# Kernel optimization log

Measured on AMD Instinct MI355X. Metric: run time of the kernel, lower is better.

## Reference

```python
import jax, jax.numpy as jnp
import numpy as np

DELTA = 0.2  # margin from __init__
EPS = 1e-8   # torch cosine_similarity eps


def setup_inputs() -> dict:
    key = jax.random.key(0)
    k1, k2, k3 = jax.random.split(key, 3)
    B, D, N = 4096, 1024, 8192
    return {
        "q": jax.random.normal(k1, (B, D), dtype=jnp.float32),
        "k": jax.random.normal(k2, (B, D), dtype=jnp.float32),
        "queue": jax.random.normal(k3, (N, D), dtype=jnp.float32),
    }


def _l2_normalize(x):
    # matches torch cosine_similarity clamping: norm clamped to eps
    n = jnp.maximum(jnp.linalg.norm(x, axis=-1, keepdims=True), EPS)
    return x / n


def reference(q, k, queue):
    qn = _l2_normalize(q)          # [B, D]
    kn = _l2_normalize(k)          # [B, D]
    queuen = _l2_normalize(queue)  # [N, D]
    pos = jnp.sum(qn * kn, axis=-1)                 # [B] cos(q_i, k_i)
    neg = jnp.einsum("bd,nd->bn", qn, queuen)       # [B, N] cos(q_i, queue_j)
    hinge = jax.nn.relu(DELTA - pos[:, None] + neg)  # [B, N]
    return jnp.sum(hinge)
```

## Files before the change

kernel.cpp:

```cpp
#include <hip/hip_runtime.h>

#define B_ROWS 4096
#define N_ROWS 8192
#define DDIM   1024
#define DELTA_M 0.2f
#define EPSF    1e-8f

#define BM 128
#define BN 128
#define BK 32

typedef short bf16x8 __attribute__((ext_vector_type(8)));
typedef float f32x4 __attribute__((ext_vector_type(4)));

__device__ inline unsigned short f32_to_bf16(float f) {
    unsigned int u = __float_as_uint(f);
    u += 0x7FFFu + ((u >> 16) & 1u);
    return (unsigned short)(u >> 16);
}

__device__ inline void load_lds16(const void* g, void* l) {
    __builtin_amdgcn_global_load_lds(
        (const __attribute__((address_space(1))) void*)g,
        (__attribute__((address_space(3))) void*)l,
        16, 0, 0);
}

__global__ __launch_bounds__(256)
void norm_kernel(const float* __restrict__ q, const float* __restrict__ k,
                 const float* __restrict__ queue,
                 unsigned short* __restrict__ qn,
                 unsigned short* __restrict__ qun,
                 float* __restrict__ pos) {
    const int tid  = threadIdx.x;
    const int lane = tid & 63;
    const int wave = tid >> 6;
    const int row  = blockIdx.x * 4 + wave;

    if (row < B_ROWS) {
        const float4* qr = reinterpret_cast<const float4*>(q + (size_t)row * DDIM);
        const float4* kr = reinterpret_cast<const float4*>(k + (size_t)row * DDIM);
        float4 a[4], b[4];
        #pragma unroll
        for (int j = 0; j < 4; ++j) a[j] = qr[lane + j * 64];
        #pragma unroll
        for (int j = 0; j < 4; ++j) b[j] = kr[lane + j * 64];
        float s11 = 0.f, s22 = 0.f, s12 = 0.f;
        #pragma unroll
        for (int j = 0; j < 4; ++j) {
            s11 += a[j].x * a[j].x + a[j].y * a[j].y + a[j].z * a[j].z + a[j].w * a[j].w;
            s22 += b[j].x * b[j].x + b[j].y * b[j].y + b[j].z * b[j].z + b[j].w * b[j].w;
            s12 += a[j].x * b[j].x + a[j].y * b[j].y + a[j].z * b[j].z + a[j].w * b[j].w;
        }
        #pragma unroll
        for (int off = 1; off < 64; off <<= 1) {
            s11 += __shfl_xor(s11, off);
            s22 += __shfl_xor(s22, off);
            s12 += __shfl_xor(s12, off);
        }
        const float inv1 = 1.0f / fmaxf(sqrtf(s11), EPSF);
        const float inv2 = 1.0f / fmaxf(sqrtf(s22), EPSF);
        if (lane == 0) pos[row] = s12 * inv1 * inv2;
        ushort4* orow = reinterpret_cast<ushort4*>(qn + (size_t)row * DDIM);
        #pragma unroll
        for (int j = 0; j < 4; ++j) {
            ushort4 o;
            o.x = f32_to_bf16(a[j].x * inv1);
            o.y = f32_to_bf16(a[j].y * inv1);
            o.z = f32_to_bf16(a[j].z * inv1);
            o.w = f32_to_bf16(a[j].w * inv1);
            orow[lane + j * 64] = o;
        }
    } else {
        const int r2 = row - B_ROWS;
        const float4* qr = reinterpret_cast<const float4*>(queue + (size_t)r2 * DDIM);
        float4 a[4];
        #pragma unroll
        for (int j = 0; j < 4; ++j) a[j] = qr[lane + j * 64];
        float s11 = 0.f;
        #pragma unroll
        for (int j = 0; j < 4; ++j)
            s11 += a[j].x * a[j].x + a[j].y * a[j].y + a[j].z * a[j].z + a[j].w * a[j].w;
        #pragma unroll
        for (int off = 1; off < 64; off <<= 1) s11 += __shfl_xor(s11, off);
        const float inv1 = 1.0f / fmaxf(sqrtf(s11), EPSF);
        ushort4* orow = reinterpret_cast<ushort4*>(qun + (size_t)r2 * DDIM);
        #pragma unroll
        for (int j = 0; j < 4; ++j) {
            ushort4 o;
            o.x = f32_to_bf16(a[j].x * inv1);
            o.y = f32_to_bf16(a[j].y * inv1);
            o.z = f32_to_bf16(a[j].z * inv1);
            o.w = f32_to_bf16(a[j].w * inv1);
            orow[lane + j * 64] = o;
        }
    }
}

__global__ __launch_bounds__(256, 2)
void gemm_hinge(const unsigned short* __restrict__ A,
                const unsigned short* __restrict__ Bq,
                const float* __restrict__ pos,
                float* __restrict__ out) {
    __shared__ unsigned short lA[BM * BK];
    __shared__ unsigned short lB[BN * BK];
    __shared__ float rbuf[4];

    const int tid  = threadIdx.x;
    const int lane = tid & 63;
    const int wave = tid >> 6;

    const int nBM = B_ROWS / BM;
    const int bid = blockIdx.x;
    const int cpx = gridDim.x >> 3;
    const int swz = (bid & 7) * cpx + (bid >> 3);
    const int bm = (swz % nBM) * BM;
    const int bn = (swz / nBM) * BN;

    const int wm = wave >> 1;
    const int wn = wave & 1;

    f32x4 acc[4][4];
    #pragma unroll
    for (int m = 0; m < 4; ++m)
        #pragma unroll
        for (int n = 0; n < 4; ++n)
            acc[m][n] = (f32x4){0.f, 0.f, 0.f, 0.f};

    const int r = tid >> 2;
    const int c = tid & 3;
    const unsigned short* gA0 = A  + (size_t)(bm + r)      * DDIM + c * 8;
    const unsigned short* gA1 = A  + (size_t)(bm + r + 64) * DDIM + c * 8;
    const unsigned short* gB0 = Bq + (size_t)(bn + r)      * DDIM + c * 8;
    const unsigned short* gB1 = Bq + (size_t)(bn + r + 64) * DDIM + c * 8;
    unsigned short* lA0 = lA + tid * 8;
    unsigned short* lA1 = lA + 64 * BK + tid * 8;
    unsigned short* lB0 = lB + tid * 8;
    unsigned short* lB1 = lB + 64 * BK + tid * 8;

    const int arow = wm * 64 + (lane & 15);
    const int brow = wn * 64 + (lane & 15);
    const int kgrp = (lane >> 4) * 8;

    for (int k0 = 0; k0 < DDIM; k0 += BK) {
        load_lds16(gA0 + k0, lA0);
        load_lds16(gA1 + k0, lA1);
        load_lds16(gB0 + k0, lB0);
        load_lds16(gB1 + k0, lB1);
        __syncthreads();
        bf16x8 af[4], bf[4];
        #pragma unroll
        for (int m = 0; m < 4; ++m)
            af[m] = *reinterpret_cast<const bf16x8*>(&lA[(arow + m * 16) * BK + kgrp]);
        #pragma unroll
        for (int n = 0; n < 4; ++n)
            bf[n] = *reinterpret_cast<const bf16x8*>(&lB[(brow + n * 16) * BK + kgrp]);
        #pragma unroll
        for (int m = 0; m < 4; ++m)
            #pragma unroll
            for (int n = 0; n < 4; ++n)
                acc[m][n] = __builtin_amdgcn_mfma_f32_16x16x32_bf16(af[m], bf[n], acc[m][n], 0, 0, 0);
        __syncthreads();
    }

    float lsum = 0.f;
    const int rj = (lane >> 4) << 2;
    #pragma unroll
    for (int m = 0; m < 4; ++m) {
        float p[4];
        #pragma unroll
        for (int j = 0; j < 4; ++j)
            p[j] = pos[bm + wm * 64 + m * 16 + rj + j];
        #pragma unroll
        for (int n = 0; n < 4; ++n)
            #pragma unroll
            for (int j = 0; j < 4; ++j)
                lsum += fmaxf(DELTA_M - p[j] + acc[m][n][j], 0.f);
    }
    #pragma unroll
    for (int off = 32; off; off >>= 1) lsum += __shfl_down(lsum, off);
    if (lane == 0) rbuf[wave] = lsum;
    __syncthreads();
    if (tid == 0) atomicAdd(out, rbuf[0] + rbuf[1] + rbuf[2] + rbuf[3]);
}

extern "C" void kernel_launch(void* const* d_in, const int* in_sizes, int n_in,
                              void* d_out, int out_size, void* d_ws, size_t ws_size,
                              hipStream_t stream) {
    const float* q     = (const float*)d_in[0];
    const float* k     = (const float*)d_in[1];
    const float* queue = (const float*)d_in[2];
    float* out = (float*)d_out;

    unsigned short* qn  = (unsigned short*)d_ws;
    unsigned short* qun = qn + (size_t)B_ROWS * DDIM;
    float* pos = (float*)(qun + (size_t)N_ROWS * DDIM);

    hipMemsetAsync(d_out, 0, sizeof(float), stream);
    norm_kernel<<<(B_ROWS + N_ROWS) / 4, 256, 0, stream>>>(q, k, queue, qn, qun, pos);
    gemm_hinge<<<(B_ROWS / BM) * (N_ROWS / BN), 256, 0, stream>>>(qn, qun, pos, out);
}
```

Before: 183.9 us.

## Double-buffer LDS tiles with global_load_lds prefetch two steps ahead

The GEMM main loop now uses two LDS buffers per operand and issues the global-to-LDS loads for tile t+2 right after the fragments for tile t are read into registers. Explicit vmcnt/lgkmcnt waits and raw s_barrier calls replace the two __syncthreads per iteration, so MFMA work overlaps the next tile's memory traffic. This doubles LDS usage, which could limit occupancy, and the hand-placed waitcnt logic must be exactly right to avoid races.

```diff
diff --git a/kernel.cpp b/kernel.cpp
--- a/kernel.cpp
+++ b/kernel.cpp
@@ -9,6 +9,7 @@
 #define BM 128
 #define BN 128
 #define BK 32
+#define NT (DDIM / BK)
 
 typedef short bf16x8 __attribute__((ext_vector_type(8)));
 typedef float f32x4 __attribute__((ext_vector_type(4)));
@@ -102,8 +103,8 @@
                 const unsigned short* __restrict__ Bq,
                 const float* __restrict__ pos,
                 float* __restrict__ out) {
-    __shared__ unsigned short lA[BM * BK];
-    __shared__ unsigned short lB[BN * BK];
+    __shared__ unsigned short lA[2 * BM * BK];
+    __shared__ unsigned short lB[2 * BN * BK];
     __shared__ float rbuf[4];
 
     const int tid  = threadIdx.x;
@@ -133,34 +134,74 @@
     const unsigned short* gA1 = A  + (size_t)(bm + r + 64) * DDIM + c * 8;
     const unsigned short* gB0 = Bq + (size_t)(bn + r)      * DDIM + c * 8;
     const unsigned short* gB1 = Bq + (size_t)(bn + r + 64) * DDIM + c * 8;
-    unsigned short* lA0 = lA + tid * 8;
-    unsigned short* lA1 = lA + 64 * BK + tid * 8;
-    unsigned short* lB0 = lB + tid * 8;
-    unsigned short* lB1 = lB + 64 * BK + tid * 8;
 
     const int arow = wm * 64 + (lane & 15);
     const int brow = wn * 64 + (lane & 15);
     const int kgrp = (lane >> 4) * 8;
 
-    for (int k0 = 0; k0 < DDIM; k0 += BK) {
-        load_lds16(gA0 + k0, lA0);
-        load_lds16(gA1 + k0, lA1);
-        load_lds16(gB0 + k0, lB0);
-        load_lds16(gB1 + k0, lB1);
-        __syncthreads();
+    {
+        unsigned short* dA = lA;
+        unsigned short* dB = lB;
+        load_lds16(gA0, dA + tid * 8);
+        load_lds16(gA1, dA + 64 * BK + tid * 8);
+        load_lds16(gB0, dB + tid * 8);
+        load_lds16(gB1, dB + 64 * BK + tid * 8);
+        dA = lA + BM * BK;
+        dB = lB + BN * BK;
+        load_lds16(gA0 + BK, dA + tid * 8);
+        load_lds16(gA1 + BK, dA + 64 * BK + tid * 8);
+        load_lds16(gB0 + BK, dB + tid * 8);
+        load_lds16(gB1 + BK, dB + 64 * BK + tid * 8);
+    }
+    asm volatile("s_waitcnt vmcnt(4)" ::: "memory");
+    __builtin_amdgcn_sched_barrier(0);
+    __builtin_amdgcn_s_barrier();
+    __builtin_amdgcn_sched_barrier(0);
+
+    for (int t = 0; t < NT; ++t) {
+        const int cur = t & 1;
+        const unsigned short* lAc = lA + cur * (BM * BK);
+        const unsigned short* lBc = lB + cur * (BN * BK);
+
         bf16x8 af[4], bf[4];
         #pragma unroll
         for (int m = 0; m < 4; ++m)
-            af[m] = *reinterpret_cast<const bf16x8*>(&lA[(arow + m * 16) * BK + kgrp]);
+            af[m] = *reinterpret_cast<const bf16x8*>(&lAc[(arow + m * 16) * BK + kgrp]);
         #pragma unroll
         for (int n = 0; n < 4; ++n)
-            bf[n] = *reinterpret_cast<const bf16x8*>(&lB[(brow + n * 16) * BK + kgrp]);
+            bf[n] = *reinterpret_cast<const bf16x8*>(&lBc[(brow + n * 16) * BK + kgrp]);
+
+        asm volatile("s_waitcnt lgkmcnt(0)" ::: "memory");
+        __builtin_amdgcn_sched_barrier(0);
+        __builtin_amdgcn_s_barrier();
+        __builtin_amdgcn_sched_barrier(0);
+
+        if (t + 2 < NT) {
+            const int k0 = (t + 2) * BK;
+            unsigned short* dA = lA + cur * (BM * BK);
+            unsigned short* dB = lB + cur * (BN * BK);
+            load_lds16(gA0 + k0, dA + tid * 8);
+            load_lds16(gA1 + k0, dA + 64 * BK + tid * 8);
+            load_lds16(gB0 + k0, dB + tid * 8);
+            load_lds16(gB1 + k0, dB + 64 * BK + tid * 8);
+        }
+
         #pragma unroll
         for (int m = 0; m < 4; ++m)
             #pragma unroll
             for (int n = 0; n < 4; ++n)
                 acc[m][n] = __builtin_amdgcn_mfma_f32_16x16x32_bf16(af[m], bf[n], acc[m][n], 0, 0, 0);
-        __syncthreads();
+
+        if (t < NT - 1) {
+            if (t + 2 < NT) {
+                asm volatile("s_waitcnt vmcnt(4)" ::: "memory");
+            } else {
+                asm volatile("s_waitcnt vmcnt(0)" ::: "memory");
+            }
+            __builtin_amdgcn_sched_barrier(0);
+            __builtin_amdgcn_s_barrier();
+            __builtin_amdgcn_sched_barrier(0);
+        }
     }
 
     float lsum = 0.f;
```

After: 179.4 us. 1.02x faster.

## Rewrite GEMM as 256x256 tile, 8-wave, double-buffered pipelined MFMA kernel

Applied to the files above, without the earlier changes.

Replaces the 128x128, single-buffered GEMM with a 256x256 block tile run by 512 threads, each wave computing four sub-quadrants. Global-to-LDS loads are double-buffered over BK=64 and interleaved with MFMA phases, with explicit vmcnt waits, barriers and setprio. LDS addresses get an XOR swizzle to avoid bank conflicts. The aim is more data reuse per load and hiding memory latency behind compute. It needs 128KB of LDS per block, which limits occupancy, and the hand-counted waits are fragile.

```diff
diff --git a/kernel.cpp b/kernel.cpp
--- a/kernel.cpp
+++ b/kernel.cpp
@@ -6,9 +6,8 @@
 #define DELTA_M 0.2f
 #define EPSF    1e-8f
 
-#define BM 128
-#define BN 128
-#define BK 32
+#define BK2 64
+#define NT2 (DDIM / BK2)
 
 typedef short bf16x8 __attribute__((ext_vector_type(8)));
 typedef float f32x4 __attribute__((ext_vector_type(4)));
@@ -24,6 +23,15 @@
         (const __attribute__((address_space(1))) void*)g,
         (__attribute__((address_space(3))) void*)l,
         16, 0, 0);
+}
+
+template<int N> __device__ __forceinline__ void vmwait() {
+    if constexpr (N == 10) asm volatile("s_waitcnt vmcnt(10)" ::: "memory");
+    else if constexpr (N == 8) asm volatile("s_waitcnt vmcnt(8)" ::: "memory");
+    else if constexpr (N == 4) asm volatile("s_waitcnt vmcnt(4)" ::: "memory");
+    else if constexpr (N == 2) asm volatile("s_waitcnt vmcnt(2)" ::: "memory");
+    else asm volatile("s_waitcnt vmcnt(0)" ::: "memory");
+    __builtin_amdgcn_sched_barrier(0);
 }
 
 __global__ __launch_bounds__(256)
@@ -97,91 +105,209 @@
     }
 }
 
-__global__ __launch_bounds__(256, 2)
+__device__ __forceinline__ void stage2(const unsigned short* M, int rowBase, int k0,
+                                       unsigned char* region,
+                                       int sr0, int sc0, int sr1, int sc1, int t16) {
+    load_lds16(M + (size_t)(rowBase + sr0) * DDIM + k0 + sc0, region + t16);
+    load_lds16(M + (size_t)(rowBase + sr1) * DDIM + k0 + sc1, region + 8192 + t16);
+}
+
+template<bool S1, bool S2, int WP0, int WP1, int WNEXT>
+__device__ __forceinline__ void gemm_window(
+    int T, unsigned char* lds,
+    const unsigned short* A, const unsigned short* Bq,
+    int bm, int bn, int wr, int wc, int aLane,
+    int sr0, int sc0, int sr1, int sc1, int t16,
+    f32x4 (&acc)[2][2][4][2]) {
+
+    const int par = T & 1;
+    const int pA0 = par * 32768;
+    const int pA1 = pA0 + 16384;
+    const int pB0 = 65536 + par * 32768;
+    const int pB1 = pB0 + 16384;
+
+    bf16x8 a[4][2], b0[2][2], b1[2][2];
+
+    #pragma unroll
+    for (int fm = 0; fm < 4; ++fm)
+        #pragma unroll
+        for (int ks = 0; ks < 2; ++ks)
+            a[fm][ks] = *reinterpret_cast<const bf16x8*>(
+                &lds[pA0 + wr * 8192 + fm * 2048 + ks * 64 + aLane]);
+    #pragma unroll
+    for (int fn = 0; fn < 2; ++fn)
+        #pragma unroll
+        for (int ks = 0; ks < 2; ++ks)
+            b0[fn][ks] = *reinterpret_cast<const bf16x8*>(
+                &lds[pB0 + wc * 4096 + fn * 2048 + ks * 64 + aLane]);
+    if (S1)
+        stage2(A, bm + 128, (T + 1) * BK2, lds + ((par ^ 1) * 32768 + 16384),
+               sr0, sc0, sr1, sc1, t16);
+    __builtin_amdgcn_s_barrier();
+    asm volatile("s_waitcnt lgkmcnt(0)" ::: "memory");
+    __builtin_amdgcn_sched_barrier(0);
+    __builtin_amdgcn_s_setprio(1);
+    #pragma unroll
+    for (int fm = 0; fm < 4; ++fm)
+        #pragma unroll
+        for (int fn = 0; fn < 2; ++fn)
+            #pragma unroll
+            for (int ks = 0; ks < 2; ++ks)
+                acc[0][0][fm][fn] = __builtin_amdgcn_mfma_f32_16x16x32_bf16(
+                    a[fm][ks], b0[fn][ks], acc[0][0][fm][fn], 0, 0, 0);
+    __builtin_amdgcn_s_setprio(0);
+    vmwait<WP0>();
+    __builtin_amdgcn_s_barrier();
+
+    #pragma unroll
+    for (int fn = 0; fn < 2; ++fn)
+        #pragma unroll
+        for (int ks = 0; ks < 2; ++ks)
+            b1[fn][ks] = *reinterpret_cast<const bf16x8*>(
+                &lds[pB1 + wc * 4096 + fn * 2048 + ks * 64 + aLane]);
+    if (S2)
+        stage2(A, bm, (T + 2) * BK2, lds + pA0, sr0, sc0, sr1, sc1, t16);
+    __builtin_amdgcn_s_barrier();
+    asm volatile("s_waitcnt lgkmcnt(0)" ::: "memory");
+    __builtin_amdgcn_sched_barrier(0);
+    __builtin_amdgcn_s_setprio(1);
+    #pragma unroll
+    for (int fm = 0; fm < 4; ++fm)
+        #pragma unroll
+        for (int fn = 0; fn < 2; ++fn)
+            #pragma unroll
+            for (int ks = 0; ks < 2; ++ks)
+                acc[0][1][fm][fn] = __builtin_amdgcn_mfma_f32_16x16x32_bf16(
+                    a[fm][ks], b1[fn][ks], acc[0][1][fm][fn], 0, 0, 0);
+    __builtin_amdgcn_s_setprio(0);
+    vmwait<WP1>();
+    __builtin_amdgcn_s_barrier();
+
+    #pragma unroll
+    for (int fm = 0; fm < 4; ++fm)
+        #pragma unroll
+        for (int ks = 0; ks < 2; ++ks)
+            a[fm][ks] = *reinterpret_cast<const bf16x8*>(
+                &lds[pA1 + wr * 8192 + fm * 2048 + ks * 64 + aLane]);
+    if (S2)
+        stage2(Bq, bn, (T + 2) * BK2, lds + pB0, sr0, sc0, sr1, sc1, t16);
+    __builtin_amdgcn_s_barrier();
+    asm volatile("s_waitcnt lgkmcnt(0)" ::: "memory");
+    __builtin_amdgcn_sched_barrier(0);
+    __builtin_amdgcn_s_setprio(1);
+    #pragma unroll
+    for (int fm = 0; fm < 4; ++fm)
+        #pragma unroll
+        for (int fn = 0; fn < 2; ++fn)
+            #pragma unroll
+            for (int ks = 0; ks < 2; ++ks)
+                acc[1][1][fm][fn] = __builtin_amdgcn_mfma_f32_16x16x32_bf16(
+                    a[fm][ks], b1[fn][ks], acc[1][1][fm][fn], 0, 0, 0);
+    __builtin_amdgcn_s_setprio(0);
+    __builtin_amdgcn_s_barrier();
+
+    if (S2)
+        stage2(Bq, bn + 128, (T + 2) * BK2, lds + pB1, sr0, sc0, sr1, sc1, t16);
+    __builtin_amdgcn_s_barrier();
+    __builtin_amdgcn_s_setprio(1);
+    #pragma unroll
+    for (int fm = 0; fm < 4; ++fm)
+        #pragma unroll
+        for (int fn = 0; fn < 2; ++fn)
+            #pragma unroll
+            for (int ks = 0; ks < 2; ++ks)
+                acc[1][0][fm][fn] = __builtin_amdgcn_mfma_f32_16x16x32_bf16(
+                    a[fm][ks], b0[fn][ks], acc[1][0][fm][fn], 0, 0, 0);
+    __builtin_amdgcn_s_setprio(0);
+    vmwait<WNEXT>();
+    __builtin_amdgcn_s_barrier();
+}
+
+__global__ __launch_bounds__(512, 2)
 void gemm_hinge(const unsigned short* __restrict__ A,
                 const unsigned short* __restrict__ Bq,
                 const float* __restrict__ pos,
                 float* __restrict__ out) {
-    __shared__ unsigned short lA[BM * BK];
-    __shared__ unsigned short lB[BN * BK];
-    __shared__ float rbuf[4];
+    __shared__ __align__(16) unsigned char lds[131072];
 
     const int tid  = threadIdx.x;
     const int lane = tid & 63;
     const int wave = tid >> 6;
 
-    const int nBM = B_ROWS / BM;
     const int bid = blockIdx.x;
-    const int cpx = gridDim.x >> 3;
-    const int swz = (bid & 7) * cpx + (bid >> 3);
-    const int bm = (swz % nBM) * BM;
-    const int bn = (swz / nBM) * BN;
-
-    const int wm = wave >> 1;
-    const int wn = wave & 1;
-
-    f32x4 acc[4][4];
-    #pragma unroll
-    for (int m = 0; m < 4; ++m)
-        #pragma unroll
-        for (int n = 0; n < 4; ++n)
-            acc[m][n] = (f32x4){0.f, 0.f, 0.f, 0.f};
-
-    const int r = tid >> 2;
-    const int c = tid & 3;
-    const unsigned short* gA0 = A  + (size_t)(bm + r)      * DDIM + c * 8;
-    const unsigned short* gA1 = A  + (size_t)(bm + r + 64) * DDIM + c * 8;
-    const unsigned short* gB0 = Bq + (size_t)(bn + r)      * DDIM + c * 8;
-    const unsigned short* gB1 = Bq + (size_t)(bn + r + 64) * DDIM + c * 8;
-    unsigned short* lA0 = lA + tid * 8;
-    unsigned short* lA1 = lA + 64 * BK + tid * 8;
-    unsigned short* lB0 = lB + tid * 8;
-    unsigned short* lB1 = lB + 64 * BK + tid * 8;
-
-    const int arow = wm * 64 + (lane & 15);
-    const int brow = wn * 64 + (lane & 15);
-    const int kgrp = (lane >> 4) * 8;
-
-    for (int k0 = 0; k0 < DDIM; k0 += BK) {
-        load_lds16(gA0 + k0, lA0);
-        load_lds16(gA1 + k0, lA1);
-        load_lds16(gB0 + k0, lB0);
-        load_lds16(gB1 + k0, lB1);
-        __syncthreads();
-        bf16x8 af[4], bf[4];
-        #pragma unroll
-        for (int m = 0; m < 4; ++m)
-            af[m] = *reinterpret_cast<const bf16x8*>(&lA[(arow + m * 16) * BK + kgrp]);
-        #pragma unroll
-        for (int n = 0; n < 4; ++n)
-            bf[n] = *reinterpret_cast<const bf16x8*>(&lB[(brow + n * 16) * BK + kgrp]);
-        #pragma unroll
-        for (int m = 0; m < 4; ++m)
-            #pragma unroll
-            for (int n = 0; n < 4; ++n)
-                acc[m][n] = __builtin_amdgcn_mfma_f32_16x16x32_bf16(af[m], bf[n], acc[m][n], 0, 0, 0);
-        __syncthreads();
+    const int swz = (bid & 7) * (gridDim.x >> 3) + (bid >> 3);
+    const int bm = (swz & 15) * 256;
+    const int bn = (swz >> 4) * 256;
+
+    const int wr = wave >> 2, wc = wave & 3;
+    const int ln15 = lane & 15, kq = lane >> 4;
+    const int aLane = (ln15 * 128 + kq * 16) ^ ((((ln15 >> 2) & 1)) << 5);
+    const int t16 = tid * 16;
+    const int d0 = t16, d1 = t16 + 8192;
+    const int l0 = d0 ^ (((d0 >> 9) & 1) << 5);
+    const int l1 = d1 ^ (((d1 >> 9) & 1) << 5);
+    const int sr0 = l0 >> 7, sc0 = (l0 & 127) >> 1;
+    const int sr1 = l1 >> 7, sc1 = (l1 & 127) >> 1;
+
+    f32x4 acc[2][2][4][2];
+    #pragma unroll
+    for (int a = 0; a < 2; ++a)
+        #pragma unroll
+        for (int b = 0; b < 2; ++b)
+            #pragma unroll
+            for (int c = 0; c < 4; ++c)
+                #pragma unroll
+                for (int d = 0; d < 2; ++d)
+                    acc[a][b][c][d] = (f32x4){0.f, 0.f, 0.f, 0.f};
+
+    stage2(A,  bm,       0,   lds,                         sr0, sc0, sr1, sc1, t16);
+    stage2(Bq, bn,       0,   lds + 65536,                 sr0, sc0, sr1, sc1, t16);
+    stage2(Bq, bn + 128, 0,   lds + 65536 + 16384,         sr0, sc0, sr1, sc1, t16);
+    stage2(A,  bm + 128, 0,   lds + 16384,                 sr0, sc0, sr1, sc1, t16);
+    stage2(A,  bm,       BK2, lds + 32768,                 sr0, sc0, sr1, sc1, t16);
+    stage2(Bq, bn,       BK2, lds + 65536 + 32768,         sr0, sc0, sr1, sc1, t16);
+    stage2(Bq, bn + 128, BK2, lds + 65536 + 32768 + 16384, sr0, sc0, sr1, sc1, t16);
+    vmwait<10>();
+    __builtin_amdgcn_s_barrier();
+
+    #pragma unroll 1
+    for (int T = 0; T < 14; ++T)
+        gemm_window<true, true, 10, 10, 10>(T, lds, A, Bq, bm, bn, wr, wc, aLane,
+                                            sr0, sc0, sr1, sc1, t16, acc);
+    gemm_window<true, false, 10, 8, 4>(14, lds, A, Bq, bm, bn, wr, wc, aLane,
+                                       sr0, sc0, sr1, sc1, t16, acc);
+    gemm_window<false, false, 2, 0, 0>(15, lds, A, Bq, bm, bn, wr, wc, aLane,
+                                       sr0, sc0, sr1, sc1, t16, acc);
+
+    float lsum = 0.f;
+    const int rj = kq * 4;
+    #pragma unroll
+    for (int mh = 0; mh < 2; ++mh)
+        #pragma unroll
+        for (int fm = 0; fm < 4; ++fm) {
+            const float4 p4 = *reinterpret_cast<const float4*>(
+                pos + bm + mh * 128 + wr * 64 + fm * 16 + rj);
+            const float pj[4] = {p4.x, p4.y, p4.z, p4.w};
+            #pragma unroll
+            for (int nh = 0; nh < 2; ++nh)
+                #pragma unroll
+                for (int fn = 0; fn < 2; ++fn)
+                    #pragma unroll
+                    for (int j = 0; j < 4; ++j)
+                        lsum += fmaxf(DELTA_M - pj[j] + acc[mh][nh][fm][fn][j], 0.f);
+        }
+    #pragma unroll
+    for (int off = 32; off; off >>= 1) lsum += __shfl_down(lsum, off);
+    __syncthreads();
+    float* red = reinterpret_cast<float*>(lds);
+    if (lane == 0) red[wave] = lsum;
+    __syncthreads();
+    if (tid == 0) {
+        float s = 0.f;
+        #pragma unroll
+        for (int w = 0; w < 8; ++w) s += red[w];
+        atomicAdd(out, s);
     }
-
-    float lsum = 0.f;
-    const int rj = (lane >> 4) << 2;
-    #pragma unroll
-    for (int m = 0; m < 4; ++m) {
-        float p[4];
-        #pragma unroll
-        for (int j = 0; j < 4; ++j)
-            p[j] = pos[bm + wm * 64 + m * 16 + rj + j];
-        #pragma unroll
-        for (int n = 0; n < 4; ++n)
-            #pragma unroll
-            for (int j = 0; j < 4; ++j)
-                lsum += fmaxf(DELTA_M - p[j] + acc[m][n][j], 0.f);
-    }
-    #pragma unroll
-    for (int off = 32; off; off >>= 1) lsum += __shfl_down(lsum, off);
-    if (lane == 0) rbuf[wave] = lsum;
-    __syncthreads();
-    if (tid == 0) atomicAdd(out, rbuf[0] + rbuf[1] + rbuf[2] + rbuf[3]);
 }
 
 extern "C" void kernel_launch(void* const* d_in, const int* in_sizes, int n_in,
@@ -198,5 +324,5 @@
 
     hipMemsetAsync(d_out, 0, sizeof(float), stream);
     norm_kernel<<<(B_ROWS + N_ROWS) / 4, 256, 0, stream>>>(q, k, queue, qn, qun, pos);
-    gemm_hinge<<<(B_ROWS / BM) * (N_ROWS / BN), 256, 0, stream>>>(qn, qun, pos, out);
-}
+    gemm_hinge<<<(B_ROWS / 256) * (N_ROWS / 256), 512, 0, stream>>>(qn, qun, pos, out);
+}
```

Measured after the change: 163.3 us. 1.13x faster.

## Rewrite GEMM as 256x256 tiles with double-buffered swizzled LDS pipeline

Applied to the files above, without the earlier changes.

The GEMM block tile grows from 128x128 to 256x256 with 16 waves. Global-to-LDS loads are double-buffered so the next K slab is staged while MFMAs run, using explicit waitcnt and barriers, and LDS addresses are XOR-swizzled to avoid bank conflicts. The output memset is folded into the norm kernel, which removes one launch. This raises arithmetic intensity and overlaps memory with compute, but it risks lower occupancy and a subtle race on the zeroing of the output.

```diff
diff --git a/kernel.cpp b/kernel.cpp
--- a/kernel.cpp
+++ b/kernel.cpp
@@ -6,9 +6,8 @@
 #define DELTA_M 0.2f
 #define EPSF    1e-8f
 
-#define BM 128
-#define BN 128
-#define BK 32
+#define BK3 32
+#define NW  (DDIM / BK3)
 
 typedef short bf16x8 __attribute__((ext_vector_type(8)));
 typedef float f32x4 __attribute__((ext_vector_type(4)));
@@ -31,11 +30,12 @@
                  const float* __restrict__ queue,
                  unsigned short* __restrict__ qn,
                  unsigned short* __restrict__ qun,
-                 float* __restrict__ pos) {
+                 float* __restrict__ pos, float* __restrict__ out) {
     const int tid  = threadIdx.x;
     const int lane = tid & 63;
     const int wave = tid >> 6;
     const int row  = blockIdx.x * 4 + wave;
+    if (blockIdx.x == 0 && tid == 0) *out = 0.f;
 
     if (row < B_ROWS) {
         const float4* qr = reinterpret_cast<const float4*>(q + (size_t)row * DDIM);
@@ -97,91 +97,126 @@
     }
 }
 
-__global__ __launch_bounds__(256, 2)
+__device__ __forceinline__ void stage_pair(const unsigned short* srcA,
+                                           const unsigned short* srcB,
+                                           int k0, unsigned char* bufA, int t16) {
+    load_lds16(srcA + k0, bufA + t16);
+    load_lds16(srcB + k0, bufA + 16384 + t16);
+}
+
+template<bool STG, int WE>
+__device__ __forceinline__ void gemm_window(
+    int T, unsigned char* lds,
+    const unsigned short* srcA, const unsigned short* srcB,
+    int aBase, int bBase, int t16, f32x4 (&acc)[4][4]) {
+
+    const int par = T & 1;
+    unsigned char* buf = lds + par * 32768;
+
+    bf16x8 a[4], b[4];
+    #pragma unroll
+    for (int fm = 0; fm < 4; ++fm)
+        a[fm] = *reinterpret_cast<const bf16x8*>(&buf[aBase + fm * 1024]);
+    #pragma unroll
+    for (int fn = 0; fn < 4; ++fn)
+        b[fn] = *reinterpret_cast<const bf16x8*>(&buf[16384 + bBase + fn * 1024]);
+    asm volatile("s_waitcnt lgkmcnt(0)" ::: "memory");
+    __builtin_amdgcn_sched_barrier(0);
+    __builtin_amdgcn_s_barrier();
+
+    if (STG)
+        stage_pair(srcA, srcB, (T + 2) * BK3, buf, t16);
+
+    __builtin_amdgcn_s_setprio(1);
+    #pragma unroll
+    for (int fm = 0; fm < 4; ++fm)
+        #pragma unroll
+        for (int fn = 0; fn < 4; ++fn)
+            acc[fm][fn] = __builtin_amdgcn_mfma_f32_16x16x32_bf16(
+                a[fm], b[fn], acc[fm][fn], 0, 0, 0);
+    __builtin_amdgcn_s_setprio(0);
+
+    if (WE >= 0) {
+        if (WE == 2)      asm volatile("s_waitcnt vmcnt(2)" ::: "memory");
+        else              asm volatile("s_waitcnt vmcnt(0)" ::: "memory");
+        __builtin_amdgcn_sched_barrier(0);
+        __builtin_amdgcn_s_barrier();
+    }
+}
+
+__global__ __launch_bounds__(1024, 4)
 void gemm_hinge(const unsigned short* __restrict__ A,
                 const unsigned short* __restrict__ Bq,
                 const float* __restrict__ pos,
                 float* __restrict__ out) {
-    __shared__ unsigned short lA[BM * BK];
-    __shared__ unsigned short lB[BN * BK];
-    __shared__ float rbuf[4];
+    __shared__ __align__(16) unsigned char lds[65536];
 
     const int tid  = threadIdx.x;
     const int lane = tid & 63;
     const int wave = tid >> 6;
 
-    const int nBM = B_ROWS / BM;
     const int bid = blockIdx.x;
-    const int cpx = gridDim.x >> 3;
-    const int swz = (bid & 7) * cpx + (bid >> 3);
-    const int bm = (swz % nBM) * BM;
-    const int bn = (swz / nBM) * BN;
-
-    const int wm = wave >> 1;
-    const int wn = wave & 1;
+    const int x   = bid & 7;
+    const int idx = bid >> 3;
+    const int bm = ((x & 1) * 8 + (idx & 7)) * 256;
+    const int bn = ((x >> 1) * 8 + (idx >> 3)) * 256;
+
+    const int wr = wave >> 2, wc = wave & 3;
+    const int ln15 = lane & 15, kq = lane >> 4;
+    const int kqoff = (kq * 16) ^ (((ln15 >> 1) & 3) << 4);
+    const int aBase = (wr * 64 + ln15) * 64 + kqoff;
+    const int bBase = (wc * 64 + ln15) * 64 + kqoff;
+
+    const int t16 = tid * 16;
+    const int l   = t16 ^ (((t16 >> 7) & 3) << 4);
+    const int sr  = l >> 6;
+    const int sc  = (l & 63) >> 1;
+    const unsigned short* srcA = A  + (size_t)(bm + sr) * DDIM + sc;
+    const unsigned short* srcB = Bq + (size_t)(bn + sr) * DDIM + sc;
 
     f32x4 acc[4][4];
     #pragma unroll
-    for (int m = 0; m < 4; ++m)
-        #pragma unroll
-        for (int n = 0; n < 4; ++n)
-            acc[m][n] = (f32x4){0.f, 0.f, 0.f, 0.f};
-
-    const int r = tid >> 2;
-    const int c = tid & 3;
-    const unsigned short* gA0 = A  + (size_t)(bm + r)      * DDIM + c * 8;
-    const unsigned short* gA1 = A  + (size_t)(bm + r + 64) * DDIM + c * 8;
-    const unsigned short* gB0 = Bq + (size_t)(bn + r)      * DDIM + c * 8;
-    const unsigned short* gB1 = Bq + (size_t)(bn + r + 64) * DDIM + c * 8;
-    unsigned short* lA0 = lA + tid * 8;
-    unsigned short* lA1 = lA + 64 * BK + tid * 8;
-    unsigned short* lB0 = lB + tid * 8;
-    unsigned short* lB1 = lB + 64 * BK + tid * 8;
-
-    const int arow = wm * 64 + (lane & 15);
-    const int brow = wn * 64 + (lane & 15);
-    const int kgrp = (lane >> 4) * 8;
-
-    for (int k0 = 0; k0 < DDIM; k0 += BK) {
-        load_lds16(gA0 + k0, lA0);
-        load_lds16(gA1 + k0, lA1);
-        load_lds16(gB0 + k0, lB0);
-        load_lds16(gB1 + k0, lB1);
-        __syncthreads();
-        bf16x8 af[4], bf[4];
-        #pragma unroll
-        for (int m = 0; m < 4; ++m)
-            af[m] = *reinterpret_cast<const bf16x8*>(&lA[(arow + m * 16) * BK + kgrp]);
-        #pragma unroll
-        for (int n = 0; n < 4; ++n)
-            bf[n] = *reinterpret_cast<const bf16x8*>(&lB[(brow + n * 16) * BK + kgrp]);
-        #pragma unroll
-        for (int m = 0; m < 4; ++m)
-            #pragma unroll
-            for (int n = 0; n < 4; ++n)
-                acc[m][n] = __builtin_amdgcn_mfma_f32_16x16x32_bf16(af[m], bf[n], acc[m][n], 0, 0, 0);
-        __syncthreads();
-    }
+    for (int fm = 0; fm < 4; ++fm)
+        #pragma unroll
+        for (int fn = 0; fn < 4; ++fn)
+            acc[fm][fn] = (f32x4){0.f, 0.f, 0.f, 0.f};
+
+    stage_pair(srcA, srcB, 0,   lds,         t16);
+    stage_pair(srcA, srcB, BK3, lds + 32768, t16);
+    asm volatile("s_waitcnt vmcnt(2)" ::: "memory");
+    __builtin_amdgcn_sched_barrier(0);
+    __builtin_amdgcn_s_barrier();
+
+    #pragma unroll 1
+    for (int T = 0; T < NW - 2; ++T)
+        gemm_window<true, 2>(T, lds, srcA, srcB, aBase, bBase, t16, acc);
+    gemm_window<false, 0>(NW - 2, lds, srcA, srcB, aBase, bBase, t16, acc);
+    gemm_window<false, -1>(NW - 1, lds, srcA, srcB, aBase, bBase, t16, acc);
 
     float lsum = 0.f;
-    const int rj = (lane >> 4) << 2;
-    #pragma unroll
-    for (int m = 0; m < 4; ++m) {
-        float p[4];
-        #pragma unroll
-        for (int j = 0; j < 4; ++j)
-            p[j] = pos[bm + wm * 64 + m * 16 + rj + j];
-        #pragma unroll
-        for (int n = 0; n < 4; ++n)
+    #pragma unroll
+    for (int fm = 0; fm < 4; ++fm) {
+        const float4 p4 = *reinterpret_cast<const float4*>(
+            pos + bm + wr * 64 + fm * 16 + kq * 4);
+        const float pj[4] = {p4.x, p4.y, p4.z, p4.w};
+        #pragma unroll
+        for (int fn = 0; fn < 4; ++fn)
             #pragma unroll
             for (int j = 0; j < 4; ++j)
-                lsum += fmaxf(DELTA_M - p[j] + acc[m][n][j], 0.f);
+                lsum += fmaxf(DELTA_M - pj[j] + acc[fm][fn][j], 0.f);
     }
     #pragma unroll
     for (int off = 32; off; off >>= 1) lsum += __shfl_down(lsum, off);
-    if (lane == 0) rbuf[wave] = lsum;
     __syncthreads();
-    if (tid == 0) atomicAdd(out, rbuf[0] + rbuf[1] + rbuf[2] + rbuf[3]);
+    float* red = reinterpret_cast<float*>(lds);
+    if (lane == 0) red[wave] = lsum;
+    __syncthreads();
+    if (tid == 0) {
+        float s = 0.f;
+        #pragma unroll
+        for (int w = 0; w < 16; ++w) s += red[w];
+        atomicAdd(out, s);
+    }
 }
 
 extern "C" void kernel_launch(void* const* d_in, const int* in_sizes, int n_in,
@@ -196,7 +231,6 @@
     unsigned short* qun = qn + (size_t)B_ROWS * DDIM;
     float* pos = (float*)(qun + (size_t)N_ROWS * DDIM);
 
-    hipMemsetAsync(d_out, 0, sizeof(float), stream);
-    norm_kernel<<<(B_ROWS + N_ROWS) / 4, 256, 0, stream>>>(q, k, queue, qn, qun, pos);
-    gemm_hinge<<<(B_ROWS / BM) * (N_ROWS / BN), 256, 0, stream>>>(qn, qun, pos, out);
-}
+    norm_kernel<<<(B_ROWS + N_ROWS) / 4, 256, 0, stream>>>(q, k, queue, qn, qun, pos, out);
+    gemm_hinge<<<(B_ROWS / 256) * (N_ROWS / 256), 1024, 0, stream>>>(qn, qun, pos, out);
+}
```

Result: faster. 162.7 us (-11.5%).
